# Kernel tuning notes

Hardware: AMD Instinct MI355X
Metric: run time of the kernel (lower is better)

The kernel has to match this reference:

```python
import jax, jax.numpy as jnp
import numpy as np

B, S, D, H = 2, 2048, 1024, 16
HD = D // H  # head_dim = 64


def setup_inputs() -> dict:
    key = jax.random.key(0)
    ks = jax.random.split(key, 6)
    std = 0.02
    return {
        "x": jax.random.normal(ks[0], (B, S, D), dtype=jnp.float32),
        "gamma": jnp.ones((D,), jnp.float32),
        "beta": jnp.zeros((D,), jnp.float32),
        "w_qkv": jax.random.normal(ks[1], (D, 3 * D), jnp.float32) * std,
        "b_qkv": jnp.zeros((3 * D,), jnp.float32),
        "w_out": jax.random.normal(ks[2], (D, D), jnp.float32) * std,
        "b_out": jnp.zeros((D,), jnp.float32),
        "w_gate": jax.random.normal(ks[3], (D, D), jnp.float32) * std,
        "b_gate": jnp.zeros((D,), jnp.float32),
    }


def reference(x, gamma, beta, w_qkv, b_qkv, w_out, b_out, w_gate, b_gate):
    residual = x
    # Pre-norm (LayerNorm over last dim, eps matches torch default 1e-5)
    mu = jnp.mean(x, axis=-1, keepdims=True)
    var = jnp.mean(jnp.square(x - mu), axis=-1, keepdims=True)
    xn = (x - mu) * jax.lax.rsqrt(var + 1e-5) * gamma + beta

    # Fused QKV projection: [B,S,3D] -> [B,S,3,H,HD]
    qkv = (xn @ w_qkv + b_qkv).reshape(B, S, 3, H, HD)
    q = qkv[:, :, 0].transpose(0, 2, 1, 3)  # [B,H,S,HD]
    k = qkv[:, :, 1].transpose(0, 2, 1, 3)
    v = qkv[:, :, 2].transpose(0, 2, 1, 3)

    scale = 1.0 / jnp.sqrt(jnp.float32(HD))
    scores = jnp.einsum("bhqd,bhkd->bhqk", q, k) * scale  # [B,H,S,S]
    attn = jax.nn.softmax(scores, axis=-1)  # dropout is identity in eval
    ctx = jnp.einsum("bhqk,bhkd->bhqd", attn, v)  # [B,H,S,HD]
    ctx = ctx.transpose(0, 2, 1, 3).reshape(B, S, D)

    out = ctx @ w_out + b_out
    gate = jax.nn.sigmoid(xn @ w_gate + b_gate)
    return out * gate + residual
```

## Files before the change

kernel.cpp:

```cpp
#include <hip/hip_runtime.h>

using u16 = unsigned short;
typedef __attribute__((ext_vector_type(8))) short bf16x8;
typedef __attribute__((ext_vector_type(4))) float f32x4;

constexpr int Bc = 2, Sc = 2048, Dc = 1024, Hc = 16;
constexpr int Mc = Bc * Sc;
constexpr int N3 = 3 * Dc;

__device__ __forceinline__ u16 f2bf(float f) {
  unsigned u = __float_as_uint(f);
  u += 0x7fffu + ((u >> 16) & 1u);
  return (u16)(u >> 16);
}

__device__ __forceinline__ void gload16(const void* g, void* l) {
  __builtin_amdgcn_global_load_lds(
      (const __attribute__((address_space(1))) void*)g,
      (__attribute__((address_space(3))) void*)l, 16, 0, 0);
}

__device__ __forceinline__ int swz(int row, int slot) {
  return row * 64 + ((slot ^ (row & 7)) << 3);
}

__device__ __forceinline__ void xcd_swizzle(int& bx, int& by) {
  const int nwg = gridDim.x * gridDim.y;
  const int bid = by * gridDim.x + bx;
  const int s = (bid & 7) * (nwg >> 3) + (bid >> 3);
  bx = s % gridDim.x;
  by = s / gridDim.x;
}

__global__ __launch_bounds__(256) void ln_kernel(
    const float* __restrict__ x, const float* __restrict__ gamma,
    const float* __restrict__ beta, u16* __restrict__ xn) {
  __shared__ float sred[8];
  const int row = blockIdx.x, tid = threadIdx.x;
  const float4 a = ((const float4*)(x + (size_t)row * Dc))[tid];
  float s = a.x + a.y + a.z + a.w;
  float ss = a.x * a.x + a.y * a.y + a.z * a.z + a.w * a.w;
#pragma unroll
  for (int off = 32; off; off >>= 1) {
    s += __shfl_xor(s, off, 64);
    ss += __shfl_xor(ss, off, 64);
  }
  const int wid = tid >> 6, lane = tid & 63;
  if (lane == 0) { sred[wid] = s; sred[4 + wid] = ss; }
  __syncthreads();
  s = sred[0] + sred[1] + sred[2] + sred[3];
  ss = sred[4] + sred[5] + sred[6] + sred[7];
  const float mean = s * (1.0f / Dc);
  const float rstd = rsqrtf(ss * (1.0f / Dc) - mean * mean + 1e-5f);
  const float4 g = ((const float4*)gamma)[tid];
  const float4 b = ((const float4*)beta)[tid];
  ushort4 o;
  o.x = f2bf((a.x - mean) * rstd * g.x + b.x);
  o.y = f2bf((a.y - mean) * rstd * g.y + b.y);
  o.z = f2bf((a.z - mean) * rstd * g.z + b.z);
  o.w = f2bf((a.w - mean) * rstd * g.w + b.w);
  *(ushort4*)(xn + (size_t)row * Dc + tid * 4) = o;
}

__global__ __launch_bounds__(256) void convertT(
    const float* __restrict__ W, u16* __restrict__ WT, int K, int N) {
  __shared__ float t[32][33];
  const int k0 = blockIdx.y * 32, n0 = blockIdx.x * 32;
  const int tid = threadIdx.x;
  const int r = tid >> 3, c4 = (tid & 7) << 2;
  const float4 v = *(const float4*)(W + (size_t)(k0 + r) * N + n0 + c4);
  t[r][c4 + 0] = v.x; t[r][c4 + 1] = v.y; t[r][c4 + 2] = v.z; t[r][c4 + 3] = v.w;
  __syncthreads();
  ushort4 o;
  o.x = f2bf(t[c4 + 0][r]); o.y = f2bf(t[c4 + 1][r]);
  o.z = f2bf(t[c4 + 2][r]); o.w = f2bf(t[c4 + 3][r]);
  *(ushort4*)(WT + (size_t)(n0 + r) * K + k0 + c4) = o;
}

__global__ __launch_bounds__(256) void gemm_qkv_kernel(
    const u16* __restrict__ A, const u16* __restrict__ BT,
    const float* __restrict__ bias, u16* __restrict__ Qb,
    u16* __restrict__ Kb, u16* __restrict__ VbT) {
  __shared__ __align__(16) u16 Al[128 * 64];
  __shared__ __align__(16) u16 Bl[128 * 64];
  const int tid = threadIdx.x, wv = tid >> 6, ln = tid & 63;
  int bxi = blockIdx.x, byi = blockIdx.y;
  xcd_swizzle(bxi, byi);
  const int bm = byi * 128, bn = bxi * 128;
  const int wr = (wv >> 1) * 64, wc = (wv & 1) * 64;

  f32x4 acc[4][4];
#pragma unroll
  for (int i = 0; i < 4; i++)
#pragma unroll
    for (int j = 0; j < 4; j++) acc[i][j] = f32x4{0.f, 0.f, 0.f, 0.f};

  for (int k0 = 0; k0 < Dc; k0 += 64) {
    __syncthreads();
#pragma unroll
    for (int c = 0; c < 4; c++) {
      const int ci = wv + c * 4;
      const int i = ci * 64 + ln;
      const int row = i >> 3, slot = i & 7;
      const size_t go = (size_t)row * Dc + k0 + ((slot ^ (row & 7)) << 3);
      gload16(A + (size_t)bm * Dc + go, &Al[ci * 512]);
      gload16(BT + (size_t)bn * Dc + go, &Bl[ci * 512]);
    }
    __syncthreads();
#pragma unroll
    for (int ks = 0; ks < 2; ks++) {
      bf16x8 af[4], bfr[4];
#pragma unroll
      for (int m = 0; m < 4; m++)
        af[m] = *(const bf16x8*)&Al[swz(wr + m * 16 + (ln & 15), ks * 4 + (ln >> 4))];
#pragma unroll
      for (int n = 0; n < 4; n++)
        bfr[n] = *(const bf16x8*)&Bl[swz(wc + n * 16 + (ln & 15), ks * 4 + (ln >> 4))];
#pragma unroll
      for (int m = 0; m < 4; m++)
#pragma unroll
        for (int n = 0; n < 4; n++)
          acc[m][n] = __builtin_amdgcn_mfma_f32_16x16x32_bf16(af[m], bfr[n], acc[m][n], 0, 0, 0);
    }
  }

  const int fq = ln >> 4, fr = ln & 15;
#pragma unroll
  for (int mi = 0; mi < 4; mi++) {
    const int row = bm + wr + mi * 16 + fq * 4;
    const int b = row >> 11, sl = row & 2047;
#pragma unroll
    for (int ni = 0; ni < 4; ni++) {
      const int col = bn + wc + ni * 16 + fr;
      const int which = col >> 10, h = (col >> 6) & 15, hd = col & 63;
      const int bh = b * Hc + h;
      const float bs = bias[col];
      if (which == 0) {
#pragma unroll
        for (int r = 0; r < 4; r++)
          Qb[((size_t)bh * Sc + sl + r) * 64 + hd] =
              f2bf((acc[mi][ni][r] + bs) * 0.18033688011112042f);
      } else if (which == 1) {
#pragma unroll
        for (int r = 0; r < 4; r++)
          Kb[((size_t)bh * Sc + sl + r) * 64 + hd] = f2bf(acc[mi][ni][r] + bs);
      } else {
        ushort4 st;
        st.x = f2bf(acc[mi][ni][0] + bs); st.y = f2bf(acc[mi][ni][1] + bs);
        st.z = f2bf(acc[mi][ni][2] + bs); st.w = f2bf(acc[mi][ni][3] + bs);
        *(ushort4*)&VbT[((size_t)bh * 64 + hd) * Sc + sl] = st;
      }
    }
  }
}

__global__ __launch_bounds__(128) void attn_kernel(
    const u16* __restrict__ Qb, const u16* __restrict__ Kb,
    const u16* __restrict__ VbT, u16* __restrict__ ctx) {
  __shared__ __align__(16) u16 Ks[2][64 * 64];
  __shared__ __align__(16) u16 Vs[2][64 * 64];
  __shared__ __align__(16) u16 Pl[2][32 * 64];
  const int tid = threadIdx.x, wv = tid >> 6, ln = tid & 63;
  const int qt = blockIdx.x, bh = blockIdx.y;
  const int b = bh >> 4, h = bh & 15;
  const int q0 = qt * 64 + wv * 32;
  constexpr float THR = 11.5f;

  bf16x8 qf[2][2];
#pragma unroll
  for (int a = 0; a < 2; a++)
#pragma unroll
    for (int ks = 0; ks < 2; ks++)
      qf[a][ks] = *(const bf16x8*)(Qb + ((size_t)bh * Sc + q0 + a * 16 + (ln & 15)) * 64 +
                                   (ks * 4 + (ln >> 4)) * 8);

  f32x4 O[2][4];
  float m_[2][4], l_[2][4];
#pragma unroll
  for (int a = 0; a < 2; a++)
#pragma unroll
    for (int f = 0; f < 4; f++) O[a][f] = f32x4{0.f, 0.f, 0.f, 0.f};
#pragma unroll
  for (int a = 0; a < 2; a++)
#pragma unroll
    for (int r = 0; r < 4; r++) { m_[a][r] = -1e30f; l_[a][r] = 0.f; }

  const u16* Kbase = Kb + (size_t)bh * Sc * 64;
  const u16* Vbase = VbT + (size_t)bh * 64 * Sc;
  u16* Pw = &Pl[wv][0];

  int rk[4], rv[4];
#pragma unroll
  for (int c = 0; c < 4; c++) {
    const int ci = wv * 4 + c;
    const int i = ci * 64 + ln;
    const int row = i >> 3, slot = i & 7;
    const int so = (slot ^ (row & 7)) << 3;
    rk[c] = row * 64 + so;
    rv[c] = row * Sc + so;
  }

  auto stage = [&](int buf, int kt) {
#pragma unroll
    for (int c = 0; c < 4; c++) {
      const int ci = wv * 4 + c;
      gload16(Kbase + (size_t)kt * 4096 + rk[c], &Ks[buf][ci * 512]);
      gload16(Vbase + (size_t)kt * 64 + rv[c], &Vs[buf][ci * 512]);
    }
  };

  stage(0, 0);
  asm volatile("s_waitcnt vmcnt(0)" ::: "memory");
  __syncthreads();

  for (int kt = 0; kt < Sc / 64; kt++) {
    const int cur = kt & 1;
    if (kt + 1 < Sc / 64) stage(cur ^ 1, kt + 1);

    f32x4 sf[2][4];
#pragma unroll
    for (int a = 0; a < 2; a++)
#pragma unroll
      for (int f = 0; f < 4; f++) sf[a][f] = f32x4{0.f, 0.f, 0.f, 0.f};
    __builtin_amdgcn_s_setprio(1);
#pragma unroll
    for (int f = 0; f < 4; f++)
#pragma unroll
      for (int ks = 0; ks < 2; ks++) {
        const bf16x8 kf = *(const bf16x8*)&Ks[cur][swz(f * 16 + (ln & 15), ks * 4 + (ln >> 4))];
#pragma unroll
        for (int a = 0; a < 2; a++)
          sf[a][f] = __builtin_amdgcn_mfma_f32_16x16x32_bf16(qf[a][ks], kf, sf[a][f], 0, 0, 0);
      }
    __builtin_amdgcn_s_setprio(0);

    float pm[2][4];
    bool need = false;
#pragma unroll
    for (int a = 0; a < 2; a++)
#pragma unroll
      for (int r = 0; r < 4; r++) {
        pm[a][r] = fmaxf(fmaxf(sf[a][0][r], sf[a][1][r]), fmaxf(sf[a][2][r], sf[a][3][r]));
        need |= pm[a][r] > m_[a][r] + THR;
      }
    if (__any(need)) {
#pragma unroll
      for (int a = 0; a < 2; a++)
#pragma unroll
        for (int r = 0; r < 4; r++) {
          float v = pm[a][r];
#pragma unroll
          for (int o = 1; o < 16; o <<= 1) v = fmaxf(v, __shfl_xor(v, o, 16));
          v = fmaxf(v, m_[a][r]);
          const float al = exp2f(m_[a][r] - v);
          m_[a][r] = v;
          l_[a][r] *= al;
#pragma unroll
          for (int f = 0; f < 4; f++) O[a][f][r] *= al;
        }
    }
#pragma unroll
    for (int a = 0; a < 2; a++)
#pragma unroll
      for (int f = 0; f < 4; f++)
#pragma unroll
        for (int r = 0; r < 4; r++) {
          const float p = exp2f(sf[a][f][r] - m_[a][r]);
          l_[a][r] += p;
          const int row = a * 16 + (ln >> 4) * 4 + r;
          const int key = f * 16 + (ln & 15);
          Pw[row * 64 + (key ^ ((row & 7) << 3))] = f2bf(p);
        }
    asm volatile("s_waitcnt lgkmcnt(0)" ::: "memory");

    __builtin_amdgcn_s_setprio(1);
#pragma unroll
    for (int ks = 0; ks < 2; ks++) {
      bf16x8 pa[2];
#pragma unroll
      for (int a = 0; a < 2; a++)
        pa[a] = *(const bf16x8*)&Pw[swz(a * 16 + (ln & 15), ks * 4 + (ln >> 4))];
#pragma unroll
      for (int f = 0; f < 4; f++) {
        const bf16x8 vb = *(const bf16x8*)&Vs[cur][swz(f * 16 + (ln & 15), ks * 4 + (ln >> 4))];
#pragma unroll
        for (int a = 0; a < 2; a++)
          O[a][f] = __builtin_amdgcn_mfma_f32_16x16x32_bf16(pa[a], vb, O[a][f], 0, 0, 0);
      }
    }
    __builtin_amdgcn_s_setprio(0);

    asm volatile("s_waitcnt vmcnt(0)" ::: "memory");
    __syncthreads();
  }

#pragma unroll
  for (int a = 0; a < 2; a++)
#pragma unroll
    for (int r = 0; r < 4; r++) {
      float v = l_[a][r];
#pragma unroll
      for (int o = 1; o < 16; o <<= 1) v += __shfl_xor(v, o, 16);
      l_[a][r] = 1.0f / v;
    }
#pragma unroll
  for (int a = 0; a < 2; a++)
#pragma unroll
    for (int f = 0; f < 4; f++)
#pragma unroll
      for (int r = 0; r < 4; r++) {
        const int row = q0 + a * 16 + (ln >> 4) * 4 + r;
        ctx[((size_t)b * Sc + row) * Dc + h * 64 + f * 16 + (ln & 15)] =
            f2bf(O[a][f][r] * l_[a][r]);
      }
}

__global__ __launch_bounds__(256) void final_kernel(
    const u16* __restrict__ ctx, const u16* __restrict__ xn,
    const u16* __restrict__ woutT, const u16* __restrict__ wgateT,
    const float* __restrict__ b_out, const float* __restrict__ b_gate,
    const float* __restrict__ x, float* __restrict__ out) {
  __shared__ __align__(16) u16 A1[128 * 64], A2[128 * 64];
  __shared__ __align__(16) u16 B1[64 * 64], B2[64 * 64];
  const int tid = threadIdx.x, wv = tid >> 6, ln = tid & 63;
  int bxi = blockIdx.x, byi = blockIdx.y;
  xcd_swizzle(bxi, byi);
  const int bm = byi * 128, bn = bxi * 64;
  const int wr = (wv >> 1) * 64, wc = (wv & 1) * 32;

  f32x4 ac1[4][2], ac2[4][2];
#pragma unroll
  for (int i = 0; i < 4; i++)
#pragma unroll
    for (int j = 0; j < 2; j++) {
      ac1[i][j] = f32x4{0.f, 0.f, 0.f, 0.f};
      ac2[i][j] = f32x4{0.f, 0.f, 0.f, 0.f};
    }

  for (int k0 = 0; k0 < Dc; k0 += 64) {
    __syncthreads();
#pragma unroll
    for (int c = 0; c < 4; c++) {
      const int ci = wv + c * 4;
      const int i = ci * 64 + ln;
      const int row = i >> 3, slot = i & 7;
      const size_t go = (size_t)row * Dc + k0 + ((slot ^ (row & 7)) << 3);
      gload16(ctx + (size_t)bm * Dc + go, &A1[ci * 512]);
      gload16(xn + (size_t)bm * Dc + go, &A2[ci * 512]);
    }
#pragma unroll
    for (int c = 0; c < 2; c++) {
      const int ci = wv + c * 4;
      const int i = ci * 64 + ln;
      const int row = i >> 3, slot = i & 7;
      const size_t go = (size_t)row * Dc + k0 + ((slot ^ (row & 7)) << 3);
      gload16(woutT + (size_t)bn * Dc + go, &B1[ci * 512]);
      gload16(wgateT + (size_t)bn * Dc + go, &B2[ci * 512]);
    }
    __syncthreads();
#pragma unroll
    for (int ks = 0; ks < 2; ks++) {
      bf16x8 fa1[4], fa2[4], fb1[2], fb2[2];
#pragma unroll
      for (int m = 0; m < 4; m++) {
        const int off = swz(wr + m * 16 + (ln & 15), ks * 4 + (ln >> 4));
        fa1[m] = *(const bf16x8*)&A1[off];
        fa2[m] = *(const bf16x8*)&A2[off];
      }
#pragma unroll
      for (int n = 0; n < 2; n++) {
        const int off = swz(wc + n * 16 + (ln & 15), ks * 4 + (ln >> 4));
        fb1[n] = *(const bf16x8*)&B1[off];
        fb2[n] = *(const bf16x8*)&B2[off];
      }
#pragma unroll
      for (int m = 0; m < 4; m++)
#pragma unroll
        for (int n = 0; n < 2; n++) {
          ac1[m][n] = __builtin_amdgcn_mfma_f32_16x16x32_bf16(fa1[m], fb1[n], ac1[m][n], 0, 0, 0);
          ac2[m][n] = __builtin_amdgcn_mfma_f32_16x16x32_bf16(fa2[m], fb2[n], ac2[m][n], 0, 0, 0);
        }
    }
  }

  const int fq = ln >> 4, fr = ln & 15;
#pragma unroll
  for (int m = 0; m < 4; m++)
#pragma unroll
    for (int n = 0; n < 2; n++) {
      const int col = bn + wc + n * 16 + fr;
      const float bo = b_out[col], bg = b_gate[col];
#pragma unroll
      for (int r = 0; r < 4; r++) {
        const int row = bm + wr + m * 16 + fq * 4 + r;
        const float o = ac1[m][n][r] + bo;
        const float gv = ac2[m][n][r] + bg;
        const float sig = 1.0f / (1.0f + __expf(-gv));
        out[(size_t)row * Dc + col] = o * sig + x[(size_t)row * Dc + col];
      }
    }
}

extern "C" void kernel_launch(void* const* d_in, const int* in_sizes, int n_in,
                              void* d_out, int out_size, void* d_ws, size_t ws_size,
                              hipStream_t stream) {
  const float* x = (const float*)d_in[0];
  const float* gamma = (const float*)d_in[1];
  const float* beta = (const float*)d_in[2];
  const float* w_qkv = (const float*)d_in[3];
  const float* b_qkv = (const float*)d_in[4];
  const float* w_out = (const float*)d_in[5];
  const float* b_out = (const float*)d_in[6];
  const float* w_gate = (const float*)d_in[7];
  const float* b_gate = (const float*)d_in[8];
  float* out = (float*)d_out;

  u16* xn = (u16*)d_ws;
  u16* wqkvT = xn + (size_t)Mc * Dc;
  u16* woutT = wqkvT + (size_t)N3 * Dc;
  u16* wgateT = woutT + (size_t)Dc * Dc;
  u16* Qb = wgateT + (size_t)Dc * Dc;
  u16* Kb = Qb + (size_t)Bc * Hc * Sc * 64;
  u16* VbT = Kb + (size_t)Bc * Hc * Sc * 64;
  u16* ctxb = VbT + (size_t)Bc * Hc * Sc * 64;

  ln_kernel<<<Mc, 256, 0, stream>>>(x, gamma, beta, xn);
  convertT<<<dim3(N3 / 32, Dc / 32), 256, 0, stream>>>(w_qkv, wqkvT, Dc, N3);
  convertT<<<dim3(Dc / 32, Dc / 32), 256, 0, stream>>>(w_out, woutT, Dc, Dc);
  convertT<<<dim3(Dc / 32, Dc / 32), 256, 0, stream>>>(w_gate, wgateT, Dc, Dc);
  gemm_qkv_kernel<<<dim3(N3 / 128, Mc / 128), 256, 0, stream>>>(
      xn, wqkvT, b_qkv, Qb, Kb, VbT);
  attn_kernel<<<dim3(Sc / 64, Bc * Hc), 128, 0, stream>>>(Qb, Kb, VbT, ctxb);
  final_kernel<<<dim3(Dc / 64, Mc / 128), 256, 0, stream>>>(
      ctxb, xn, woutT, wgateT, b_out, b_gate, x, out);
}
```

Before: 270.7 us.

## Transpose attention score MFMA layout and use packed bf16 conversion instructions

The score MFMA now computes K·Qᵀ so that each lane holds one query row's scores. This lets the row max and row sum be reduced in-register, with only two cross-lane shuffles per row instead of a 16-lane butterfly per element. All manual round-to-nearest bf16 conversions are replaced by the hardware v_cvt_pk_bf16_f32 instruction. P is written to LDS as packed 8-byte stores with precomputed swizzled offsets. The per-row rescale now needs a shuffle to move alpha into the output layout, and the exact layout mapping has to stay consistent.

```diff
diff --git a/kernel.cpp b/kernel.cpp
--- a/kernel.cpp
+++ b/kernel.cpp
@@ -8,10 +8,11 @@
 constexpr int Mc = Bc * Sc;
 constexpr int N3 = 3 * Dc;
 
-__device__ __forceinline__ u16 f2bf(float f) {
-  unsigned u = __float_as_uint(f);
-  u += 0x7fffu + ((u >> 16) & 1u);
-  return (u16)(u >> 16);
+__device__ __forceinline__ ushort4 pk4(float a, float b, float c, float d) {
+  union { uint2 u; ushort4 s; } r;
+  asm("v_cvt_pk_bf16_f32 %0, %1, %2" : "=v"(r.u.x) : "v"(a), "v"(b));
+  asm("v_cvt_pk_bf16_f32 %0, %1, %2" : "=v"(r.u.y) : "v"(c), "v"(d));
+  return r.s;
 }
 
 __device__ __forceinline__ void gload16(const void* g, void* l) {
@@ -54,12 +55,9 @@
   const float rstd = rsqrtf(ss * (1.0f / Dc) - mean * mean + 1e-5f);
   const float4 g = ((const float4*)gamma)[tid];
   const float4 b = ((const float4*)beta)[tid];
-  ushort4 o;
-  o.x = f2bf((a.x - mean) * rstd * g.x + b.x);
-  o.y = f2bf((a.y - mean) * rstd * g.y + b.y);
-  o.z = f2bf((a.z - mean) * rstd * g.z + b.z);
-  o.w = f2bf((a.w - mean) * rstd * g.w + b.w);
-  *(ushort4*)(xn + (size_t)row * Dc + tid * 4) = o;
+  *(ushort4*)(xn + (size_t)row * Dc + tid * 4) =
+      pk4((a.x - mean) * rstd * g.x + b.x, (a.y - mean) * rstd * g.y + b.y,
+          (a.z - mean) * rstd * g.z + b.z, (a.w - mean) * rstd * g.w + b.w);
 }
 
 __global__ __launch_bounds__(256) void convertT(
@@ -71,10 +69,8 @@
   const float4 v = *(const float4*)(W + (size_t)(k0 + r) * N + n0 + c4);
   t[r][c4 + 0] = v.x; t[r][c4 + 1] = v.y; t[r][c4 + 2] = v.z; t[r][c4 + 3] = v.w;
   __syncthreads();
-  ushort4 o;
-  o.x = f2bf(t[c4 + 0][r]); o.y = f2bf(t[c4 + 1][r]);
-  o.z = f2bf(t[c4 + 2][r]); o.w = f2bf(t[c4 + 3][r]);
-  *(ushort4*)(WT + (size_t)(n0 + r) * K + k0 + c4) = o;
+  *(ushort4*)(WT + (size_t)(n0 + r) * K + k0 + c4) =
+      pk4(t[c4 + 0][r], t[c4 + 1][r], t[c4 + 2][r], t[c4 + 3][r]);
 }
 
 __global__ __launch_bounds__(256) void gemm_qkv_kernel(
@@ -136,19 +132,20 @@
       const int bh = b * Hc + h;
       const float bs = bias[col];
       if (which == 0) {
-#pragma unroll
-        for (int r = 0; r < 4; r++)
-          Qb[((size_t)bh * Sc + sl + r) * 64 + hd] =
-              f2bf((acc[mi][ni][r] + bs) * 0.18033688011112042f);
+        constexpr float SC = 0.18033688011112042f;
+        const ushort4 s = pk4((acc[mi][ni][0] + bs) * SC, (acc[mi][ni][1] + bs) * SC,
+                              (acc[mi][ni][2] + bs) * SC, (acc[mi][ni][3] + bs) * SC);
+        u16* p = &Qb[((size_t)bh * Sc + sl) * 64 + hd];
+        p[0] = s.x; p[64] = s.y; p[128] = s.z; p[192] = s.w;
       } else if (which == 1) {
-#pragma unroll
-        for (int r = 0; r < 4; r++)
-          Kb[((size_t)bh * Sc + sl + r) * 64 + hd] = f2bf(acc[mi][ni][r] + bs);
+        const ushort4 s = pk4(acc[mi][ni][0] + bs, acc[mi][ni][1] + bs,
+                              acc[mi][ni][2] + bs, acc[mi][ni][3] + bs);
+        u16* p = &Kb[((size_t)bh * Sc + sl) * 64 + hd];
+        p[0] = s.x; p[64] = s.y; p[128] = s.z; p[192] = s.w;
       } else {
-        ushort4 st;
-        st.x = f2bf(acc[mi][ni][0] + bs); st.y = f2bf(acc[mi][ni][1] + bs);
-        st.z = f2bf(acc[mi][ni][2] + bs); st.w = f2bf(acc[mi][ni][3] + bs);
-        *(ushort4*)&VbT[((size_t)bh * 64 + hd) * Sc + sl] = st;
+        *(ushort4*)&VbT[((size_t)bh * 64 + hd) * Sc + sl] =
+            pk4(acc[mi][ni][0] + bs, acc[mi][ni][1] + bs,
+                acc[mi][ni][2] + bs, acc[mi][ni][3] + bs);
       }
     }
   }
@@ -161,33 +158,41 @@
   __shared__ __align__(16) u16 Vs[2][64 * 64];
   __shared__ __align__(16) u16 Pl[2][32 * 64];
   const int tid = threadIdx.x, wv = tid >> 6, ln = tid & 63;
+  const int g = ln >> 4, q = ln & 15;
   const int qt = blockIdx.x, bh = blockIdx.y;
   const int b = bh >> 4, h = bh & 15;
   const int q0 = qt * 64 + wv * 32;
   constexpr float THR = 11.5f;
+  const f32x4 ZZ = {0.f, 0.f, 0.f, 0.f};
 
   bf16x8 qf[2][2];
 #pragma unroll
   for (int a = 0; a < 2; a++)
 #pragma unroll
     for (int ks = 0; ks < 2; ks++)
-      qf[a][ks] = *(const bf16x8*)(Qb + ((size_t)bh * Sc + q0 + a * 16 + (ln & 15)) * 64 +
-                                   (ks * 4 + (ln >> 4)) * 8);
+      qf[a][ks] = *(const bf16x8*)(Qb + ((size_t)bh * Sc + q0 + a * 16 + q) * 64 +
+                                   (ks * 4 + g) * 8);
 
   f32x4 O[2][4];
-  float m_[2][4], l_[2][4];
 #pragma unroll
   for (int a = 0; a < 2; a++)
 #pragma unroll
-    for (int f = 0; f < 4; f++) O[a][f] = f32x4{0.f, 0.f, 0.f, 0.f};
-#pragma unroll
-  for (int a = 0; a < 2; a++)
-#pragma unroll
-    for (int r = 0; r < 4; r++) { m_[a][r] = -1e30f; l_[a][r] = 0.f; }
+    for (int f = 0; f < 4; f++) O[a][f] = ZZ;
+  float m_[2] = {-1e30f, -1e30f}, l_[2] = {0.f, 0.f};
 
   const u16* Kbase = Kb + (size_t)bh * Sc * 64;
   const u16* Vbase = VbT + (size_t)bh * 64 * Sc;
   u16* Pw = &Pl[wv][0];
+
+  int pofs[2][4];
+#pragma unroll
+  for (int a = 0; a < 2; a++)
+#pragma unroll
+    for (int f = 0; f < 4; f++) {
+      const int row = a * 16 + q;
+      const int slot = 2 * f + (g >> 1);
+      pofs[a][f] = row * 64 + ((slot ^ (q & 7)) << 3) + (g & 1) * 4;
+    }
 
   int rk[4], rv[4];
 #pragma unroll
@@ -218,59 +223,66 @@
     if (kt + 1 < Sc / 64) stage(cur ^ 1, kt + 1);
 
     f32x4 sf[2][4];
-#pragma unroll
-    for (int a = 0; a < 2; a++)
-#pragma unroll
-      for (int f = 0; f < 4; f++) sf[a][f] = f32x4{0.f, 0.f, 0.f, 0.f};
     __builtin_amdgcn_s_setprio(1);
 #pragma unroll
-    for (int f = 0; f < 4; f++)
-#pragma unroll
-      for (int ks = 0; ks < 2; ks++) {
-        const bf16x8 kf = *(const bf16x8*)&Ks[cur][swz(f * 16 + (ln & 15), ks * 4 + (ln >> 4))];
-#pragma unroll
-        for (int a = 0; a < 2; a++)
-          sf[a][f] = __builtin_amdgcn_mfma_f32_16x16x32_bf16(qf[a][ks], kf, sf[a][f], 0, 0, 0);
-      }
+    for (int f = 0; f < 4; f++) {
+      const bf16x8 kf0 = *(const bf16x8*)&Ks[cur][swz(f * 16 + q, g)];
+      const bf16x8 kf1 = *(const bf16x8*)&Ks[cur][swz(f * 16 + q, 4 + g)];
+#pragma unroll
+      for (int a = 0; a < 2; a++) {
+        f32x4 t = __builtin_amdgcn_mfma_f32_16x16x32_bf16(kf0, qf[a][0], ZZ, 0, 0, 0);
+        sf[a][f] = __builtin_amdgcn_mfma_f32_16x16x32_bf16(kf1, qf[a][1], t, 0, 0, 0);
+      }
+    }
     __builtin_amdgcn_s_setprio(0);
 
-    float pm[2][4];
+    float pm[2];
     bool need = false;
 #pragma unroll
-    for (int a = 0; a < 2; a++)
-#pragma unroll
-      for (int r = 0; r < 4; r++) {
-        pm[a][r] = fmaxf(fmaxf(sf[a][0][r], sf[a][1][r]), fmaxf(sf[a][2][r], sf[a][3][r]));
-        need |= pm[a][r] > m_[a][r] + THR;
-      }
+    for (int a = 0; a < 2; a++) {
+      float v = fmaxf(fmaxf(sf[a][0][0], sf[a][0][1]), fmaxf(sf[a][0][2], sf[a][0][3]));
+#pragma unroll
+      for (int f = 1; f < 4; f++) {
+        v = fmaxf(v, fmaxf(fmaxf(sf[a][f][0], sf[a][f][1]), fmaxf(sf[a][f][2], sf[a][f][3])));
+      }
+      pm[a] = v;
+      need |= pm[a] > m_[a] + THR;
+    }
     if (__any(need)) {
 #pragma unroll
-      for (int a = 0; a < 2; a++)
+      for (int a = 0; a < 2; a++) {
+        float v = pm[a];
+        v = fmaxf(v, __shfl_xor(v, 16));
+        v = fmaxf(v, __shfl_xor(v, 32));
+        v = fmaxf(v, m_[a]);
+        const float al = exp2f(m_[a] - v);
+        m_[a] = v;
+        l_[a] *= al;
 #pragma unroll
         for (int r = 0; r < 4; r++) {
-          float v = pm[a][r];
-#pragma unroll
-          for (int o = 1; o < 16; o <<= 1) v = fmaxf(v, __shfl_xor(v, o, 16));
-          v = fmaxf(v, m_[a][r]);
-          const float al = exp2f(m_[a][r] - v);
-          m_[a][r] = v;
-          l_[a][r] *= al;
-#pragma unroll
-          for (int f = 0; f < 4; f++) O[a][f][r] *= al;
+          const float alo = __shfl(al, g * 4 + r);
+#pragma unroll
+          for (int f = 0; f < 4; f++) O[a][f][r] *= alo;
         }
-    }
-#pragma unroll
-    for (int a = 0; a < 2; a++)
-#pragma unroll
-      for (int f = 0; f < 4; f++)
-#pragma unroll
-        for (int r = 0; r < 4; r++) {
-          const float p = exp2f(sf[a][f][r] - m_[a][r]);
-          l_[a][r] += p;
-          const int row = a * 16 + (ln >> 4) * 4 + r;
-          const int key = f * 16 + (ln & 15);
-          Pw[row * 64 + (key ^ ((row & 7) << 3))] = f2bf(p);
-        }
+      }
+    }
+#pragma unroll
+    for (int a = 0; a < 2; a++) {
+      float linc = 0.f;
+#pragma unroll
+      for (int f = 0; f < 4; f++) {
+        const float p0 = exp2f(sf[a][f][0] - m_[a]);
+        const float p1 = exp2f(sf[a][f][1] - m_[a]);
+        const float p2 = exp2f(sf[a][f][2] - m_[a]);
+        const float p3 = exp2f(sf[a][f][3] - m_[a]);
+        linc += (p0 + p1) + (p2 + p3);
+        uint2 pk;
+        asm("v_cvt_pk_bf16_f32 %0, %1, %2" : "=v"(pk.x) : "v"(p0), "v"(p1));
+        asm("v_cvt_pk_bf16_f32 %0, %1, %2" : "=v"(pk.y) : "v"(p2), "v"(p3));
+        *(uint2*)&Pw[pofs[a][f]] = pk;
+      }
+      l_[a] += linc;
+    }
     asm volatile("s_waitcnt lgkmcnt(0)" ::: "memory");
 
     __builtin_amdgcn_s_setprio(1);
@@ -279,10 +291,10 @@
       bf16x8 pa[2];
 #pragma unroll
       for (int a = 0; a < 2; a++)
-        pa[a] = *(const bf16x8*)&Pw[swz(a * 16 + (ln & 15), ks * 4 + (ln >> 4))];
+        pa[a] = *(const bf16x8*)&Pw[swz(a * 16 + q, ks * 4 + g)];
 #pragma unroll
       for (int f = 0; f < 4; f++) {
-        const bf16x8 vb = *(const bf16x8*)&Vs[cur][swz(f * 16 + (ln & 15), ks * 4 + (ln >> 4))];
+        const bf16x8 vb = *(const bf16x8*)&Vs[cur][swz(f * 16 + q, ks * 4 + g)];
 #pragma unroll
         for (int a = 0; a < 2; a++)
           O[a][f] = __builtin_amdgcn_mfma_f32_16x16x32_bf16(pa[a], vb, O[a][f], 0, 0, 0);
@@ -295,24 +307,26 @@
   }
 
 #pragma unroll
+  for (int a = 0; a < 2; a++) {
+    l_[a] += __shfl_xor(l_[a], 16);
+    l_[a] += __shfl_xor(l_[a], 32);
+  }
+  float linv[2][4];
+#pragma unroll
   for (int a = 0; a < 2; a++)
 #pragma unroll
-    for (int r = 0; r < 4; r++) {
-      float v = l_[a][r];
-#pragma unroll
-      for (int o = 1; o < 16; o <<= 1) v += __shfl_xor(v, o, 16);
-      l_[a][r] = 1.0f / v;
-    }
+    for (int r = 0; r < 4; r++)
+      linv[a][r] = 1.0f / __shfl(l_[a], g * 4 + r);
+
 #pragma unroll
   for (int a = 0; a < 2; a++)
 #pragma unroll
-    for (int f = 0; f < 4; f++)
-#pragma unroll
-      for (int r = 0; r < 4; r++) {
-        const int row = q0 + a * 16 + (ln >> 4) * 4 + r;
-        ctx[((size_t)b * Sc + row) * Dc + h * 64 + f * 16 + (ln & 15)] =
-            f2bf(O[a][f][r] * l_[a][r]);
-      }
+    for (int f = 0; f < 4; f++) {
+      const ushort4 s = pk4(O[a][f][0] * linv[a][0], O[a][f][1] * linv[a][1],
+                            O[a][f][2] * linv[a][2], O[a][f][3] * linv[a][3]);
+      u16* p = ctx + ((size_t)b * Sc + q0 + a * 16 + g * 4) * Dc + h * 64 + f * 16 + q;
+      p[0] = s.x; p[Dc] = s.y; p[2 * Dc] = s.z; p[3 * Dc] = s.w;
+    }
 }
 
 __global__ __launch_bounds__(256) void final_kernel(
```

Measured after the change: 251.5 us. -7.1%, faster.
